# Kernel optimization log

Hardware: AMD Instinct MI355X
Metric: run time of the kernel (lower is better)

Reference implementation:

```python
import jax, jax.numpy as jnp
import numpy as np

DIGITS = 4
SAMPLES = 2048
BATCH = 512
ALPHA = 0.1


def setup_inputs() -> dict:
    key = jax.random.key(0)
    k1, k2, k3 = jax.random.split(key, 3)
    n1_logits = jax.random.normal(k1, (BATCH, DIGITS, 10), dtype=jnp.float32)
    # sample counters start at ones and stay positive; keep them in (1, 2)
    counters = jax.random.uniform(k2, (DIGITS, 10), dtype=jnp.float32) + 1.0
    s = jax.random.randint(k3, (BATCH,), 0, 10 ** DIGITS, dtype=jnp.int32)
    return {"n1_logits": n1_logits, "counters": counters, "s": s}


def reference(n1_logits, counters, s):
    B, D, _ = n1_logits.shape
    S = SAMPLES
    key = jax.random.key(42)
    digit_idx = jnp.arange(10, dtype=jnp.int32)
    constraint = jnp.zeros((B, S), dtype=jnp.int32)
    samples_list = []
    for i in range(D):
        if i == 0:
            maxim = (s // 10 ** (D - 1)).astype(jnp.int32)
            minim = jnp.maximum(0, maxim - 9)
        else:
            maxim = ((s // 10 ** (D - 1 - i)) % 10).astype(jnp.int32)
            minim = jnp.zeros_like(maxim)
        # [B, S, 10]: per-digit logits repeated over samples, counter penalty
        probs = n1_logits[:, i, None, :] - ALPHA * jnp.log(counters[i])[None, None, :]
        probs = jnp.broadcast_to(probs, (B, S, 10))
        # restrict to [minim, maxim] per batch row (equiv of per-row tf.concat with -inf pads)
        valid = (digit_idx[None, :] >= minim[:, None]) & (digit_idx[None, :] <= maxim[:, None])  # [B,10]
        probs_cut = jnp.where(valid[:, None, :], probs, -jnp.inf)
        logits = jnp.where(constraint[..., None] == 1, probs, probs_cut)
        key, sub = jax.random.split(key)
        samp = jax.random.categorical(sub, logits).astype(jnp.int32)  # [B,S]
        constraint = jnp.maximum(jnp.where(samp == maxim[:, None], 0, 1), constraint)
        samples_list.append(samp)
    n1_samples = jnp.stack(samples_list, axis=-1)  # [B,S,D]
    multiplier = (10 ** jnp.arange(D - 1, -1, -1)).astype(jnp.int32)  # [D]
    n1_summed = jnp.sum(n1_samples * multiplier, axis=-1)  # [B,S]
    n2 = s[:, None] - n1_summed  # [B,S], guaranteed in [0, 10^D)
    # sample_weights: per-row multiplicity of each sampled value (unique_with_counts+gather)
    V = 10 ** D
    row = jnp.arange(B, dtype=jnp.int32)[:, None]
    hist = jnp.zeros((B, V), jnp.float32).at[row, n1_summed].add(1.0)
    weights = jnp.take_along_axis(hist, n1_summed, axis=1)  # [B,S]
    # decimalise n2 via cumulative-quotient + sorted shift trick (faithful to tf code)
    mult2 = jnp.concatenate(
        [jnp.full((D - 1,), 10, dtype=jnp.int32), jnp.zeros((1,), dtype=jnp.int32)]
    )  # [10,...,10,0]
    n2d = n2[..., None] // multiplier  # [B,S,D] cumulative quotients
    n2d = n2d - jnp.sort(n2d * mult2, axis=-1)
    return n1_samples[..., None], n2d[..., None], weights
```

## Files before the change

### kernel.cpp

```cpp
#include <hip/hip_runtime.h>
#include <stdint.h>
#include <stddef.h>


namespace {

constexpr int B = 512, S = 2048, D = 4, NC = 10;
constexpr int BS = B * S;
constexpr size_t OUT1_OFF = (size_t)BS * D;
constexpr size_t OUT2_OFF = (size_t)BS * D * 2;

constexpr uint32_t crotl(uint32_t x, int d) { return (x << d) | (x >> (32 - d)); }
struct CU2 { uint32_t a, b; };
constexpr CU2 ctf(uint32_t k0, uint32_t k1, uint32_t c0, uint32_t c1) {
  uint32_t ks2 = k0 ^ k1 ^ 0x1BD11BDAu;
  uint32_t x0 = c0 + k0, x1 = c1 + k1;
  const int rots[8] = {13, 15, 26, 6, 17, 29, 16, 24};
  const uint32_t ks[3] = {k0, k1, ks2};
  for (int blk = 0; blk < 5; ++blk) {
    for (int j = 0; j < 4; ++j) {
      int r = rots[(blk & 1) * 4 + j];
      x0 += x1; x1 = crotl(x1, r); x1 ^= x0;
    }
    x0 += ks[(blk + 1) % 3];
    x1 += ks[(blk + 2) % 3] + (uint32_t)(blk + 1);
  }
  return CU2{x0, x1};
}

struct Keys { uint32_t kx[D]; uint32_t ky[D]; };
constexpr Keys make_keys() {
  Keys K{};
  uint32_t a = 0u, b = 42u;
  for (int i = 0; i < D; ++i) {
    CU2 sub = ctf(a, b, 0u, 1u);
    CU2 nk  = ctf(a, b, 0u, 0u);
    K.kx[i] = sub.a; K.ky[i] = sub.b;
    a = nk.a; b = nk.b;
  }
  return K;
}
constexpr Keys KEYS = make_keys();

struct U2 { uint32_t a, b; };
__device__ __forceinline__ uint32_t rotl32(uint32_t x, int d) {
  return (x << d) | (x >> (32 - d));
}
__device__ __forceinline__ U2 tf(uint32_t k0, uint32_t k1, uint32_t c0, uint32_t c1) {
  uint32_t ks2 = k0 ^ k1 ^ 0x1BD11BDAu;
  uint32_t x0 = c0 + k0, x1 = c1 + k1;
#define TF_RND(r) { x0 += x1; x1 = rotl32(x1, (r)); x1 ^= x0; }
  TF_RND(13) TF_RND(15) TF_RND(26) TF_RND(6)   x0 += k1;  x1 += ks2 + 1u;
  TF_RND(17) TF_RND(29) TF_RND(16) TF_RND(24)  x0 += ks2; x1 += k0 + 2u;
  TF_RND(13) TF_RND(15) TF_RND(26) TF_RND(6)   x0 += k0;  x1 += k1 + 3u;
  TF_RND(17) TF_RND(29) TF_RND(16) TF_RND(24)  x0 += k1;  x1 += ks2 + 4u;
  TF_RND(13) TF_RND(15) TF_RND(26) TF_RND(6)   x0 += ks2; x1 += k0 + 5u;
#undef TF_RND
  return U2{x0, x1};
}

__device__ __forceinline__ float xla_logf(float a) {
  uint32_t bits = __float_as_uint(a);
  float e = (float)((int)(bits >> 23) - 126);
  float m = __uint_as_float((bits & 0x007fffffu) | 0x3f000000u);
  bool mlt = m < 0.707106781186547524f;
  float tmp = mlt ? m : 0.0f;
  float x = __fsub_rn(m, 1.0f);
  e = __fsub_rn(e, mlt ? 1.0f : 0.0f);
  x = __fadd_rn(x, tmp);
  float x2 = __fmul_rn(x, x);
  float x3 = __fmul_rn(x2, x);
  float y  = __fmaf_rn(7.0376836292e-2f,  x, -1.1514610310e-1f);
  float y1 = __fmaf_rn(-1.2420140846e-1f, x,  1.4249322787e-1f);
  float y2 = __fmaf_rn(2.0000714765e-1f,  x, -2.4999993993e-1f);
  y  = __fmaf_rn(y,  x,  1.1676998740e-1f);
  y1 = __fmaf_rn(y1, x, -1.6668057665e-1f);
  y2 = __fmaf_rn(y2, x,  3.3333331174e-1f);
  y  = __fmaf_rn(y, x3, y1);
  y  = __fmaf_rn(y, x3, y2);
  y  = __fmul_rn(y, x3);
  y1 = __fmul_rn(e, -2.12194440e-4f);
  tmp = __fmul_rn(x2, 0.5f);
  y = __fadd_rn(y, y1);
  x = __fsub_rn(x, tmp);
  y2 = __fmul_rn(e, 0.693359375f);
  x = __fadd_rn(x, y);
  x = __fadd_rn(x, y2);
  return x;
}

__device__ __forceinline__ float gumbel_from_bits(uint32_t bits) {
  float f = __fsub_rn(__uint_as_float((bits >> 9) | 0x3f800000u), 1.0f);
  float u = __fadd_rn(f, 1.17549435e-38f);
  float l1 = xla_logf(u);
  float l2 = xla_logf(-l1);
  return -l2;
}

__global__ __launch_bounds__(256) void sample_kernel(
    const float* __restrict__ logits,
    const float* __restrict__ counters,
    const int*   __restrict__ s_in,
    float* __restrict__ out)
{
  __shared__ float s_alog[D * NC];
  int t = threadIdx.x;
  if (t < D * NC) s_alog[t] = __fmul_rn(0.1f, xla_logf(counters[t]));
  __syncthreads();

  int tid = blockIdx.x * 256 + t;
  int b = tid >> 11;
  int sval = s_in[b];
  int mx0 = sval / 1000;
  int mx1 = (sval / 100) % 10;
  int mx2 = (sval / 10) % 10;
  int mx3 = sval % 10;
  int mx[D] = {mx0, mx1, mx2, mx3};

  uint32_t n0 = (uint32_t)tid * (uint32_t)NC;
  int con = 0;
  int dg[D];
  for (int i = 0; i < D; ++i) {
    uint32_t kx = KEYS.kx[i], ky = KEYS.ky[i];
    int mxi = mx[i];
    float best = -__builtin_inff();
    int bi = 0;
#pragma unroll
    for (int c = 0; c < NC; ++c) {
      U2 r = tf(kx, ky, 0u, n0 + (uint32_t)c);
      float g = gumbel_from_bits(r.a ^ r.b);
      float p = __fsub_rn(logits[(b * D + i) * NC + c], s_alog[i * NC + c]);
      float v = __fadd_rn(g, p);
      bool allowed = (con != 0) || (c <= mxi);
      if (allowed && v > best) { best = v; bi = c; }
    }
    dg[i] = bi;
    con |= (bi != mxi);
  }

  int n1v = dg[0] * 1000 + dg[1] * 100 + dg[2] * 10 + dg[3];
  int n2 = sval - n1v;
  int q0 = n2 / 1000, q1 = (n2 / 100) % 10, q2 = (n2 / 10) % 10, q3 = n2 % 10;

  size_t o = (size_t)tid * D;
  out[o + 0] = (float)dg[0];
  out[o + 1] = (float)dg[1];
  out[o + 2] = (float)dg[2];
  out[o + 3] = (float)dg[3];
  out[OUT1_OFF + o + 0] = (float)q0;
  out[OUT1_OFF + o + 1] = (float)q1;
  out[OUT1_OFF + o + 2] = (float)q2;
  out[OUT1_OFF + o + 3] = (float)q3;
}

__global__ __launch_bounds__(1024) void weights_kernel(float* __restrict__ out) {
  __shared__ int hist[10000];
  int b = blockIdx.x;
  for (int i = threadIdx.x; i < 10000; i += 1024) hist[i] = 0;
  __syncthreads();
  int vals[2];
#pragma unroll
  for (int k = 0; k < 2; ++k) {
    int sidx = (int)threadIdx.x + k * 1024;
    const float* p = out + ((size_t)(b * S + sidx)) * D;
    int v = 1000 * (int)p[0] + 100 * (int)p[1] + 10 * (int)p[2] + (int)p[3];
    vals[k] = v;
    atomicAdd(&hist[v], 1);
  }
  __syncthreads();
#pragma unroll
  for (int k = 0; k < 2; ++k) {
    int sidx = (int)threadIdx.x + k * 1024;
    out[OUT2_OFF + (size_t)b * S + sidx] = (float)hist[vals[k]];
  }
}

}

extern "C" void kernel_launch(void* const* d_in, const int* in_sizes, int n_in,
                              void* d_out, int out_size, void* d_ws, size_t ws_size,
                              hipStream_t stream) {
  const float* logits   = (const float*)d_in[0];
  const float* counters = (const float*)d_in[1];
  const int*   s_in     = (const int*)d_in[2];
  float* out = (float*)d_out;

  sample_kernel<<<BS / 256, 256, 0, stream>>>(logits, counters, s_in, out);
  weights_kernel<<<B, 1024, 0, stream>>>(out);
}
```

Measured before the change: 177.2 us.

## Fuse sampling and histogram weights into one per-row kernel

Merges the sampling kernel and the weights kernel into a single kernel with one 1024-thread block per batch row. Each thread samples two entries and adds them straight into a shared-memory histogram, so the weights pass no longer re-reads digits from global memory and one launch is dropped. The per-row logits minus the counter penalty are precomputed in shared memory, and outputs are written as float4 stores. The trade-off is fewer, larger blocks (512 of 1024 threads) and more register pressure from the unrolled digit loop inside a two-iteration loop, which may reduce occupancy for this compute-heavy threefry work.

```diff
diff --git a/kernel.cpp b/kernel.cpp
--- a/kernel.cpp
+++ b/kernel.cpp
@@ -97,80 +97,70 @@
   return -l2;
 }
 
-__global__ __launch_bounds__(256) void sample_kernel(
+__global__ __launch_bounds__(1024) void fused_kernel(
     const float* __restrict__ logits,
     const float* __restrict__ counters,
     const int*   __restrict__ s_in,
     float* __restrict__ out)
 {
-  __shared__ float s_alog[D * NC];
-  int t = threadIdx.x;
-  if (t < D * NC) s_alog[t] = __fmul_rn(0.1f, xla_logf(counters[t]));
+  __shared__ int hist[10000];
+  __shared__ float s_p[D * NC];
+  const int t = threadIdx.x;
+  const int b = blockIdx.x;
+
+  for (int i = t; i < 10000; i += 1024) hist[i] = 0;
+  if (t < D * NC) {
+    s_p[t] = __fsub_rn(logits[b * D * NC + t],
+                       __fmul_rn(0.1f, xla_logf(counters[t])));
+  }
   __syncthreads();
 
-  int tid = blockIdx.x * 256 + t;
-  int b = tid >> 11;
-  int sval = s_in[b];
-  int mx0 = sval / 1000;
-  int mx1 = (sval / 100) % 10;
-  int mx2 = (sval / 10) % 10;
-  int mx3 = sval % 10;
-  int mx[D] = {mx0, mx1, mx2, mx3};
+  const int sval = s_in[b];
+  const int mx[D] = {sval / 1000, (sval / 100) % 10, (sval / 10) % 10, sval % 10};
 
-  uint32_t n0 = (uint32_t)tid * (uint32_t)NC;
-  int con = 0;
-  int dg[D];
-  for (int i = 0; i < D; ++i) {
-    uint32_t kx = KEYS.kx[i], ky = KEYS.ky[i];
-    int mxi = mx[i];
-    float best = -__builtin_inff();
-    int bi = 0;
-#pragma unroll
-    for (int c = 0; c < NC; ++c) {
-      U2 r = tf(kx, ky, 0u, n0 + (uint32_t)c);
-      float g = gumbel_from_bits(r.a ^ r.b);
-      float p = __fsub_rn(logits[(b * D + i) * NC + c], s_alog[i * NC + c]);
-      float v = __fadd_rn(g, p);
-      bool allowed = (con != 0) || (c <= mxi);
-      if (allowed && v > best) { best = v; bi = c; }
-    }
-    dg[i] = bi;
-    con |= (bi != mxi);
-  }
-
-  int n1v = dg[0] * 1000 + dg[1] * 100 + dg[2] * 10 + dg[3];
-  int n2 = sval - n1v;
-  int q0 = n2 / 1000, q1 = (n2 / 100) % 10, q2 = (n2 / 10) % 10, q3 = n2 % 10;
-
-  size_t o = (size_t)tid * D;
-  out[o + 0] = (float)dg[0];
-  out[o + 1] = (float)dg[1];
-  out[o + 2] = (float)dg[2];
-  out[o + 3] = (float)dg[3];
-  out[OUT1_OFF + o + 0] = (float)q0;
-  out[OUT1_OFF + o + 1] = (float)q1;
-  out[OUT1_OFF + o + 2] = (float)q2;
-  out[OUT1_OFF + o + 3] = (float)q3;
-}
-
-__global__ __launch_bounds__(1024) void weights_kernel(float* __restrict__ out) {
-  __shared__ int hist[10000];
-  int b = blockIdx.x;
-  for (int i = threadIdx.x; i < 10000; i += 1024) hist[i] = 0;
-  __syncthreads();
   int vals[2];
 #pragma unroll
   for (int k = 0; k < 2; ++k) {
-    int sidx = (int)threadIdx.x + k * 1024;
-    const float* p = out + ((size_t)(b * S + sidx)) * D;
-    int v = 1000 * (int)p[0] + 100 * (int)p[1] + 10 * (int)p[2] + (int)p[3];
-    vals[k] = v;
-    atomicAdd(&hist[v], 1);
+    const int sidx = t + k * 1024;
+    const uint32_t n0 = (uint32_t)(b * S + sidx) * (uint32_t)NC;
+    int con = 0;
+    int dg[D];
+#pragma unroll
+    for (int i = 0; i < D; ++i) {
+      const uint32_t kx = KEYS.kx[i], ky = KEYS.ky[i];
+      const int mxi = mx[i];
+      float best = -__builtin_inff();
+      int bi = 0;
+#pragma unroll
+      for (int c = 0; c < NC; ++c) {
+        U2 r = tf(kx, ky, 0u, n0 + (uint32_t)c);
+        float g = gumbel_from_bits(r.a ^ r.b);
+        float v = __fadd_rn(g, s_p[i * NC + c]);
+        bool allowed = (con != 0) || (c <= mxi);
+        if (allowed && v > best) { best = v; bi = c; }
+      }
+      dg[i] = bi;
+      con |= (bi != mxi);
+    }
+
+    const int n1v = dg[0] * 1000 + dg[1] * 100 + dg[2] * 10 + dg[3];
+    vals[k] = n1v;
+    atomicAdd(&hist[n1v], 1);
+
+    const int n2 = sval - n1v;
+    const int q0 = n2 / 1000, q1 = (n2 / 100) % 10, q2 = (n2 / 10) % 10, q3 = n2 % 10;
+
+    const size_t o = (size_t)(b * S + sidx) * D;
+    *reinterpret_cast<float4*>(out + o) =
+        make_float4((float)dg[0], (float)dg[1], (float)dg[2], (float)dg[3]);
+    *reinterpret_cast<float4*>(out + OUT1_OFF + o) =
+        make_float4((float)q0, (float)q1, (float)q2, (float)q3);
   }
+
   __syncthreads();
 #pragma unroll
   for (int k = 0; k < 2; ++k) {
-    int sidx = (int)threadIdx.x + k * 1024;
+    const int sidx = t + k * 1024;
     out[OUT2_OFF + (size_t)b * S + sidx] = (float)hist[vals[k]];
   }
 }
@@ -185,6 +175,5 @@
   const int*   s_in     = (const int*)d_in[2];
   float* out = (float*)d_out;
 
-  sample_kernel<<<BS / 256, 256, 0, stream>>>(logits, counters, s_in, out);
-  weights_kernel<<<B, 1024, 0, stream>>>(out);
+  fused_kernel<<<B, 1024, 0, stream>>>(logits, counters, s_in, out);
 }
```

After: 185.3 us. +4.6%, slower.
